# Kernel tuning notes

Hardware: AMD Instinct MI355X
Metric: run time of the kernel (lower is better)

Reference implementation:

```python
import jax, jax.numpy as jnp
import numpy as np

NB_NODE = 100000
FT = 256
OUT_FT = 256
NB_REL = 4
BATCH = 8192
DEG = 16  # padded neighbors per (node, relation)


def setup_inputs() -> dict:
    key = jax.random.key(0)
    k1, k2, k3, k4 = jax.random.split(key, 4)
    features = jax.random.normal(k1, (NB_NODE, FT), dtype=jnp.float32)
    neighbor_idx = jax.random.randint(k2, (BATCH, NB_REL, DEG), 0, NB_NODE, dtype=jnp.int32)
    # per-relation GCN weight, scaled like xavier
    W = jax.random.normal(k3, (NB_REL, FT, OUT_FT), dtype=jnp.float32) * (1.0 / np.sqrt(FT))
    b = jnp.zeros((NB_REL, OUT_FT), dtype=jnp.float32)
    prelu_a = jnp.full((1,), 0.25, dtype=jnp.float32)  # nn.PReLU() default single param
    node_list = jax.random.randint(k4, (BATCH,), 0, NB_NODE, dtype=jnp.int32)
    return {"features": features, "neighbor_idx": neighbor_idx, "W": W, "b": b,
            "prelu_a": prelu_a, "node_list": node_list, "k": 0}


def _prelu(x, a):
    return jnp.where(x >= 0, x, a * x)


def reference(features, neighbor_idx, W, b, prelu_a, node_list, k):
    # Ragged per-relation neighbor gather + mean (vectorized form of the
    # python double loop): [B, R, D, F] -> mean over D -> [B, R, F]
    v_in = jnp.mean(features[neighbor_idx], axis=2)
    # Per-relation GCN linear + PReLU: [B, R, F] x [R, F, O] -> [B, R, O]
    h = jnp.einsum('brf,rfo->bro', v_in, W) + b[None, :, :]
    h = _prelu(h, prelu_a[0])
    # isAtt=False branch: mean over relations -> [B, O]
    return jnp.mean(h, axis=1)
```

## Files before the change

kernel.cpp:

```cpp
#include <hip/hip_runtime.h>
#include <hip/hip_bf16.h>

#define B_TOT 8192
#define FT    256
#define NREL  4
#define DEG   16

typedef __attribute__((ext_vector_type(8))) short bf16x8;
typedef __attribute__((ext_vector_type(4))) float f32x4;

static __device__ __forceinline__ unsigned short f2bf(float x) {
    union { float f; unsigned int u; } c; c.f = x;
    unsigned int u = c.u;
    u += 0x7fffu + ((u >> 16) & 1u);
    return (unsigned short)(u >> 16);
}
static __device__ __forceinline__ float bf2f(unsigned short h) {
    union { unsigned int u; float f; } c; c.u = ((unsigned int)h) << 16;
    return c.f;
}
static __device__ __forceinline__ int pack2(float lo, float hi) {
    return ((int)f2bf(hi) << 16) | (int)f2bf(lo);
}

__global__ __launch_bounds__(256) void cvt_feat_k(const float* __restrict__ f,
                                                  int* __restrict__ fb,
                                                  int n8) {
    int i = blockIdx.x * 256 + threadIdx.x;
    if (i < n8) {
        float4 a = ((const float4*)f)[i * 2];
        float4 b = ((const float4*)f)[i * 2 + 1];
        int4 o;
        o.x = pack2(a.x, a.y); o.y = pack2(a.z, a.w);
        o.z = pack2(b.x, b.y); o.w = pack2(b.z, b.w);
        ((int4*)fb)[i] = o;
    }
}

__global__ __launch_bounds__(256) void wtrans_k(const float* __restrict__ W,
                                                unsigned short* __restrict__ Wt) {
    __shared__ float t[64][65];
    int r = blockIdx.z, ft = blockIdx.y, ot = blockIdx.x;
    int c = threadIdx.x & 63, rw = threadIdx.x >> 6;
    const float* src = W + ((size_t)r * 256 + ft * 64) * 256 + ot * 64;
#pragma unroll
    for (int i = 0; i < 16; ++i) {
        int row = i * 4 + rw;
        t[row][c] = src[(size_t)row * 256 + c];
    }
    __syncthreads();
    unsigned short* dst = Wt + ((size_t)r * 256 + ot * 64) * 256 + ft * 64;
#pragma unroll
    for (int i = 0; i < 16; ++i) {
        int row = i * 4 + rw;
        dst[(size_t)row * 256 + c] = f2bf(t[c][row]);
    }
}

__global__ __launch_bounds__(256) void fused_k(const unsigned short* __restrict__ fb,
                                               const int* __restrict__ nidx,
                                               const unsigned short* __restrict__ Wt,
                                               const float* __restrict__ bias,
                                               const float* __restrict__ prelu,
                                               float* __restrict__ out) {
    __shared__ unsigned short A[NREL][16][264];
    int tid = threadIdx.x, lane = tid & 63, w = tid >> 6;
    int blk = blockIdx.x;

    for (int j = 0; j < 16; ++j) {
        int b = blk * 16 + j;
        const int* idx = nidx + ((size_t)b * NREL + w) * DEG;
        int4 i0 = *(const int4*)(idx);
        int4 i1 = *(const int4*)(idx + 4);
        int4 i2 = *(const int4*)(idx + 8);
        int4 i3 = *(const int4*)(idx + 12);
        float s0 = 0.f, s1 = 0.f, s2 = 0.f, s3 = 0.f;
#define ACC(nn) { const ushort4 x = ((const ushort4*)(fb + (size_t)(nn) * FT))[lane]; \
                  s0 += bf2f(x.x); s1 += bf2f(x.y); s2 += bf2f(x.z); s3 += bf2f(x.w); }
        ACC(i0.x) ACC(i0.y) ACC(i0.z) ACC(i0.w)
        ACC(i1.x) ACC(i1.y) ACC(i1.z) ACC(i1.w)
        ACC(i2.x) ACC(i2.y) ACC(i2.z) ACC(i2.w)
        ACC(i3.x) ACC(i3.y) ACC(i3.z) ACC(i3.w)
#undef ACC
        const float inv = 1.0f / 16.0f;
        ushort4 o;
        o.x = f2bf(s0 * inv); o.y = f2bf(s1 * inv);
        o.z = f2bf(s2 * inv); o.w = f2bf(s3 * inv);
        *(ushort4*)(&A[w][j][lane * 4]) = o;
    }
    __syncthreads();

    int mrow = lane & 15, quad = lane >> 4;
    float pa = prelu[0];
    f32x4 accO[4] = {};
#pragma unroll
    for (int r = 0; r < NREL; ++r) {
        f32x4 acc[4] = {};
#pragma unroll
        for (int kk = 0; kk < 8; ++kk) {
            int k0 = kk * 32 + quad * 8;
            bf16x8 a = *(const bf16x8*)&A[r][mrow][k0];
#pragma unroll
            for (int nt = 0; nt < 4; ++nt) {
                int n = w * 64 + nt * 16 + mrow;
                bf16x8 bf = *(const bf16x8*)(Wt + ((size_t)(r * 256 + n)) * 256 + k0);
                acc[nt] = __builtin_amdgcn_mfma_f32_16x16x32_bf16(a, bf, acc[nt], 0, 0, 0);
            }
        }
#pragma unroll
        for (int nt = 0; nt < 4; ++nt) {
            float bv = bias[r * 256 + w * 64 + nt * 16 + mrow];
#pragma unroll
            for (int i = 0; i < 4; ++i) {
                float h = acc[nt][i] + bv;
                h = (h >= 0.f) ? h : pa * h;
                accO[nt][i] += h;
            }
        }
    }
#pragma unroll
    for (int nt = 0; nt < 4; ++nt) {
        int ocol = w * 64 + nt * 16 + mrow;
#pragma unroll
        for (int i = 0; i < 4; ++i) {
            int row = blk * 16 + quad * 4 + i;
            out[(size_t)row * 256 + ocol] = accO[nt][i] * 0.25f;
        }
    }
}

__global__ __launch_bounds__(256) void gather_mean_k(const float* __restrict__ feat,
                                                     const int* __restrict__ nidx,
                                                     unsigned short* __restrict__ v) {
    int wave = threadIdx.x >> 6;
    int lane = threadIdx.x & 63;
    int task = blockIdx.x * 4 + wave;
    int b = task >> 2, r = task & 3;
    const int* idx = nidx + ((size_t)b * NREL + r) * DEG;
    int4 i0 = *(const int4*)(idx);
    int4 i1 = *(const int4*)(idx + 4);
    int4 i2 = *(const int4*)(idx + 8);
    int4 i3 = *(const int4*)(idx + 12);
    float4 s = make_float4(0.f, 0.f, 0.f, 0.f);
#define ACC(nn) { const float4 x = ((const float4*)(feat + (size_t)(nn) * FT))[lane]; \
                  s.x += x.x; s.y += x.y; s.z += x.z; s.w += x.w; }
    ACC(i0.x) ACC(i0.y) ACC(i0.z) ACC(i0.w)
    ACC(i1.x) ACC(i1.y) ACC(i1.z) ACC(i1.w)
    ACC(i2.x) ACC(i2.y) ACC(i2.z) ACC(i2.w)
    ACC(i3.x) ACC(i3.y) ACC(i3.z) ACC(i3.w)
#undef ACC
    const float inv = 1.0f / 16.0f;
    ushort4 o;
    o.x = f2bf(s.x * inv); o.y = f2bf(s.y * inv);
    o.z = f2bf(s.z * inv); o.w = f2bf(s.w * inv);
    *(ushort4*)(v + ((size_t)r * B_TOT + b) * FT + 4 * lane) = o;
}

__global__ __launch_bounds__(256) void gemm_k(const unsigned short* __restrict__ v,
                                              const unsigned short* __restrict__ Wt,
                                              const float* __restrict__ bias,
                                              const float* __restrict__ prelu,
                                              float* __restrict__ out) {
    __shared__ unsigned short As[64][264];
    __shared__ unsigned short Bs[64][264];
    int tid  = threadIdx.x;
    int lane = tid & 63, w = tid >> 6;
    int wm = w >> 1, wn = w & 1;
    int mrow = lane & 15, quad = lane >> 4;
    int bid = blockIdx.x;
    int m0 = (bid & 127) * 64, n0 = (bid >> 7) * 64;
    float pa = prelu[0];

    f32x4 accO[2][2] = {};
    int ocol0 = n0 + wn * 32 + mrow;

    for (int r = 0; r < NREL; ++r) {
        const unsigned short* Ag = v  + ((size_t)r * B_TOT + m0) * FT;
        const unsigned short* Bg = Wt + ((size_t)r * 256  + n0) * FT;
#pragma unroll
        for (int i = 0; i < 8; ++i) {
            int u = tid + i * 256;
            int row = u >> 5, c8 = (u & 31) * 8;
            *(int4*)(&As[row][c8]) = *(const int4*)(Ag + row * FT + c8);
            *(int4*)(&Bs[row][c8]) = *(const int4*)(Bg + row * FT + c8);
        }
        __syncthreads();

        f32x4 acc[2][2] = {};
#pragma unroll
        for (int kk = 0; kk < 8; ++kk) {
            int k0 = kk * 32 + quad * 8;
            bf16x8 a0 = *(const bf16x8*)&As[wm * 32 + mrow][k0];
            bf16x8 a1 = *(const bf16x8*)&As[wm * 32 + 16 + mrow][k0];
            bf16x8 b0 = *(const bf16x8*)&Bs[wn * 32 + mrow][k0];
            bf16x8 b1 = *(const bf16x8*)&Bs[wn * 32 + 16 + mrow][k0];
            acc[0][0] = __builtin_amdgcn_mfma_f32_16x16x32_bf16(a0, b0, acc[0][0], 0, 0, 0);
            acc[1][0] = __builtin_amdgcn_mfma_f32_16x16x32_bf16(a1, b0, acc[1][0], 0, 0, 0);
            acc[0][1] = __builtin_amdgcn_mfma_f32_16x16x32_bf16(a0, b1, acc[0][1], 0, 0, 0);
            acc[1][1] = __builtin_amdgcn_mfma_f32_16x16x32_bf16(a1, b1, acc[1][1], 0, 0, 0);
        }
        __syncthreads();

        float b0v = bias[r * 256 + ocol0];
        float b1v = bias[r * 256 + ocol0 + 16];
#pragma unroll
        for (int mt = 0; mt < 2; ++mt)
#pragma unroll
            for (int i = 0; i < 4; ++i) {
                float h0 = acc[mt][0][i] + b0v; h0 = (h0 >= 0.f) ? h0 : pa * h0;
                float h1 = acc[mt][1][i] + b1v; h1 = (h1 >= 0.f) ? h1 : pa * h1;
                accO[mt][0][i] += h0;
                accO[mt][1][i] += h1;
            }
    }

#pragma unroll
    for (int mt = 0; mt < 2; ++mt)
#pragma unroll
        for (int i = 0; i < 4; ++i) {
            int row = m0 + wm * 32 + mt * 16 + quad * 4 + i;
            out[(size_t)row * 256 + ocol0]      = accO[mt][0][i] * 0.25f;
            out[(size_t)row * 256 + ocol0 + 16] = accO[mt][1][i] * 0.25f;
        }
}

extern "C" void kernel_launch(void* const* d_in, const int* in_sizes, int n_in,
                              void* d_out, int out_size, void* d_ws, size_t ws_size,
                              hipStream_t stream) {
    const float* feat  = (const float*)d_in[0];
    const int*   nidx  = (const int*)  d_in[1];
    const float* W     = (const float*)d_in[2];
    const float* bias  = (const float*)d_in[3];
    const float* prelu = (const float*)d_in[4];
    float* out = (float*)d_out;

    const size_t feat_elems = (size_t)in_sizes[0];
    const size_t fb_bytes = feat_elems * 2;
    const size_t wt_bytes = (size_t)NREL * 256 * FT * 2;
    const size_t v_bytes  = (size_t)NREL * B_TOT * FT * 2;

    if (ws_size >= fb_bytes + wt_bytes) {
        unsigned short* fb = (unsigned short*)d_ws;
        unsigned short* Wt = fb + feat_elems;
        int n8 = (int)(feat_elems / 8);
        cvt_feat_k<<<(n8 + 255) / 256, 256, 0, stream>>>(feat, (int*)fb, n8);
        wtrans_k<<<dim3(4, 4, 4), 256, 0, stream>>>(W, Wt);
        fused_k<<<B_TOT / 16, 256, 0, stream>>>(fb, nidx, Wt, bias, prelu, out);
    } else {
        unsigned short* v  = (unsigned short*)d_ws;
        unsigned short* Wt = v + (size_t)NREL * B_TOT * FT;
        (void)v_bytes;
        wtrans_k<<<dim3(4, 4, 4), 256, 0, stream>>>(W, Wt);
        gather_mean_k<<<B_TOT, 256, 0, stream>>>(feat, nidx, v);
        gemm_k<<<512, 256, 0, stream>>>(v, Wt, bias, prelu, out);
    }
}
```

Baseline: 252.6 us.

## Use 16 waves per block in fused gather-GEMM kernel

The fused kernel grows from 4 to 16 waves per block. Each wave now gathers all four relations for one batch row, instead of one wave looping over 16 rows for a single relation. In the GEMM phase each wave computes a single 16-column output tile rather than four. The goal is more memory-level parallelism in the gather phase and more resident waves to hide latency. In exchange, each wave's MFMA loop does less work, and the larger block may limit occupancy.

```diff
diff --git a/kernel.cpp b/kernel.cpp
--- a/kernel.cpp
+++ b/kernel.cpp
@@ -57,19 +57,21 @@
     }
 }
 
-__global__ __launch_bounds__(256) void fused_k(const unsigned short* __restrict__ fb,
-                                               const int* __restrict__ nidx,
-                                               const unsigned short* __restrict__ Wt,
-                                               const float* __restrict__ bias,
-                                               const float* __restrict__ prelu,
-                                               float* __restrict__ out) {
+__global__ __launch_bounds__(1024) void fused_k(const unsigned short* __restrict__ fb,
+                                                const int* __restrict__ nidx,
+                                                const unsigned short* __restrict__ Wt,
+                                                const float* __restrict__ bias,
+                                                const float* __restrict__ prelu,
+                                                float* __restrict__ out) {
     __shared__ unsigned short A[NREL][16][264];
-    int tid = threadIdx.x, lane = tid & 63, w = tid >> 6;
+    int tid = threadIdx.x, lane = tid & 63, wv = tid >> 6;
     int blk = blockIdx.x;
-
-    for (int j = 0; j < 16; ++j) {
-        int b = blk * 16 + j;
-        const int* idx = nidx + ((size_t)b * NREL + w) * DEG;
+    int b = blk * 16 + wv;
+
+    const int* idxb = nidx + (size_t)b * NREL * DEG;
+#pragma unroll
+    for (int r = 0; r < NREL; ++r) {
+        const int* idx = idxb + r * DEG;
         int4 i0 = *(const int4*)(idx);
         int4 i1 = *(const int4*)(idx + 4);
         int4 i2 = *(const int4*)(idx + 8);
@@ -86,46 +88,37 @@
         ushort4 o;
         o.x = f2bf(s0 * inv); o.y = f2bf(s1 * inv);
         o.z = f2bf(s2 * inv); o.w = f2bf(s3 * inv);
-        *(ushort4*)(&A[w][j][lane * 4]) = o;
+        *(ushort4*)(&A[r][wv][lane * 4]) = o;
     }
     __syncthreads();
 
     int mrow = lane & 15, quad = lane >> 4;
     float pa = prelu[0];
-    f32x4 accO[4] = {};
+    int n = wv * 16 + mrow;
+    f32x4 accO = {};
 #pragma unroll
     for (int r = 0; r < NREL; ++r) {
-        f32x4 acc[4] = {};
+        f32x4 acc = {};
+        const unsigned short* Bg = Wt + ((size_t)(r * 256 + n)) * 256;
 #pragma unroll
         for (int kk = 0; kk < 8; ++kk) {
             int k0 = kk * 32 + quad * 8;
-            bf16x8 a = *(const bf16x8*)&A[r][mrow][k0];
-#pragma unroll
-            for (int nt = 0; nt < 4; ++nt) {
-                int n = w * 64 + nt * 16 + mrow;
-                bf16x8 bf = *(const bf16x8*)(Wt + ((size_t)(r * 256 + n)) * 256 + k0);
-                acc[nt] = __builtin_amdgcn_mfma_f32_16x16x32_bf16(a, bf, acc[nt], 0, 0, 0);
-            }
-        }
-#pragma unroll
-        for (int nt = 0; nt < 4; ++nt) {
-            float bv = bias[r * 256 + w * 64 + nt * 16 + mrow];
-#pragma unroll
-            for (int i = 0; i < 4; ++i) {
-                float h = acc[nt][i] + bv;
-                h = (h >= 0.f) ? h : pa * h;
-                accO[nt][i] += h;
-            }
-        }
-    }
-#pragma unroll
-    for (int nt = 0; nt < 4; ++nt) {
-        int ocol = w * 64 + nt * 16 + mrow;
+            bf16x8 a  = *(const bf16x8*)&A[r][mrow][k0];
+            bf16x8 bf = *(const bf16x8*)(Bg + k0);
+            acc = __builtin_amdgcn_mfma_f32_16x16x32_bf16(a, bf, acc, 0, 0, 0);
+        }
+        float bv = bias[r * 256 + n];
 #pragma unroll
         for (int i = 0; i < 4; ++i) {
-            int row = blk * 16 + quad * 4 + i;
-            out[(size_t)row * 256 + ocol] = accO[nt][i] * 0.25f;
-        }
+            float h = acc[i] + bv;
+            h = (h >= 0.f) ? h : pa * h;
+            accO[i] += h;
+        }
+    }
+#pragma unroll
+    for (int i = 0; i < 4; ++i) {
+        int row = blk * 16 + quad * 4 + i;
+        out[(size_t)row * 256 + n] = accO[i] * 0.25f;
     }
 }
 
@@ -237,7 +230,6 @@
     const size_t feat_elems = (size_t)in_sizes[0];
     const size_t fb_bytes = feat_elems * 2;
     const size_t wt_bytes = (size_t)NREL * 256 * FT * 2;
-    const size_t v_bytes  = (size_t)NREL * B_TOT * FT * 2;
 
     if (ws_size >= fb_bytes + wt_bytes) {
         unsigned short* fb = (unsigned short*)d_ws;
@@ -245,11 +237,10 @@
         int n8 = (int)(feat_elems / 8);
         cvt_feat_k<<<(n8 + 255) / 256, 256, 0, stream>>>(feat, (int*)fb, n8);
         wtrans_k<<<dim3(4, 4, 4), 256, 0, stream>>>(W, Wt);
-        fused_k<<<B_TOT / 16, 256, 0, stream>>>(fb, nidx, Wt, bias, prelu, out);
+        fused_k<<<B_TOT / 16, 1024, 0, stream>>>(fb, nidx, Wt, bias, prelu, out);
     } else {
         unsigned short* v  = (unsigned short*)d_ws;
         unsigned short* Wt = v + (size_t)NREL * B_TOT * FT;
-        (void)v_bytes;
         wtrans_k<<<dim3(4, 4, 4), 256, 0, stream>>>(W, Wt);
         gather_mean_k<<<B_TOT, 256, 0, stream>>>(feat, nidx, v);
         gemm_k<<<512, 256, 0, stream>>>(v, Wt, bias, prelu, out);
```

After: 231.5 us. 8.3% less time.
